# Optimization experiments

Hardware: AMD Instinct MI355X
Metric: run time of the kernel (lower is better)

## Reference

```python
import jax, jax.numpy as jnp
import numpy as np

D_MODEL = 1024
MAX_NUM_LAYERS = 4


def setup_inputs() -> dict:
    key = jax.random.key(0)
    ks = jax.random.split(key, 8)
    S, B, D, L = 1024, 2, D_MODEL, 3
    w = lambda k: (jax.random.normal(k, (D, D), dtype=jnp.float32) * 0.02)
    return {
        "x": jax.random.normal(ks[0], (S, B, D), dtype=jnp.float32),
        "layer_outputs": jax.random.normal(ks[1], (L, S, B, D), dtype=jnp.float32),
        "Wq": w(ks[2]), "bq": jnp.zeros((D,), jnp.float32),
        "Wk": w(ks[3]), "bk": jnp.zeros((D,), jnp.float32),
        "Wv": w(ks[4]), "bv": jnp.zeros((D,), jnp.float32),
        "Wo": w(ks[5]), "bo": jnp.zeros((D,), jnp.float32),
        "layer_weights": jnp.ones((MAX_NUM_LAYERS + 1,), jnp.float32),
        "num_heads": 16,
    }


def reference(x, layer_outputs, Wq, bq, Wk, bk, Wv, bv, Wo, bo, layer_weights, num_heads):
    # x: [S, B, D]; layer_outputs: [L, S, B, D] (stacked prev layer outputs)
    S, B, D = x.shape
    H = num_heads
    hd = D // H
    scale = hd ** -0.5
    # q from x only: [S, B*H, hd] -> [BH, S, hd]
    q = (x @ Wq.T + bq).reshape(S, B * H, hd).transpose(1, 0, 2)
    # k/v from x and all previous layer outputs (shared K/V projections)
    xs = jnp.concatenate([x[None], layer_outputs], axis=0)          # [Lp1, S, B, D]
    Lp1 = xs.shape[0]
    k = (xs @ Wk.T + bk).reshape(Lp1, S, B * H, hd).transpose(0, 2, 1, 3)  # [Lp1, BH, S, hd]
    v = (xs @ Wv.T + bv).reshape(Lp1, S, B * H, hd).transpose(0, 2, 1, 3)
    # per-layer scores, softmax over the key axis (torch dim=-2 of stacked scores)
    scores = jnp.einsum('bqd,lbkd->lbqk', q, k) * scale             # [Lp1, BH, S, S]
    attn = jax.nn.softmax(scores, axis=-1)
    lw = jax.nn.softmax(layer_weights[:Lp1])                        # [Lp1]
    combined = jnp.einsum('l,lbqk,lbkd->bqd', lw, attn, v)          # [BH, S, hd]
    combined = combined.transpose(1, 0, 2).reshape(S, B, D)
    return combined @ Wo.T + bo
```

## Files before the change

### kernel.cpp

```cpp
#include <hip/hip_runtime.h>
#include <hip/hip_bf16.h>
#include <math.h>

#define S_LEN   1024
#define BATCH   2
#define DMODEL  1024
#define NHEADS  16
#define HDIM    64
#define BHEADS  32
#define LP1     4
#define ROWS_PL 2048

typedef __attribute__((ext_vector_type(8)))  short bf16x8;
typedef __attribute__((ext_vector_type(4)))  float f32x4;
typedef __attribute__((ext_vector_type(16))) float f32x16;

__device__ inline ushort bf16_rne(float a) {
    unsigned u = __float_as_uint(a);
    return (ushort)((u + 0x7FFFu + ((u >> 16) & 1u)) >> 16);
}
__device__ inline float bf16_up(ushort h) { return __uint_as_float(((unsigned)h) << 16); }
__device__ inline void split_bf16(float a, ushort &hi, ushort &lo) {
    hi = bf16_rne(a);
    lo = bf16_rne(a - bf16_up(hi));
}
__device__ inline uint pk_bf16(float a, float b) {
    float2 f; f.x = a; f.y = b;
    __hip_bfloat162 h = __float22bfloat162_rn(f);
    return *reinterpret_cast<uint*>(&h);
}
#if __has_builtin(__builtin_amdgcn_exp2f)
__device__ inline float fast_exp2(float x) { return __builtin_amdgcn_exp2f(x); }
#else
__device__ inline float fast_exp2(float x) { return exp2f(x); }
#endif

__device__ inline void permswap(uint &a, uint &b) {
    asm("v_permlane32_swap_b32 %0, %1" : "+v"(a), "+v"(b));
}

__device__ inline void glds16(const ushort* g, ushort* l) {
    __builtin_amdgcn_global_load_lds(
        (const __attribute__((address_space(1))) void*)g,
        (__attribute__((address_space(3))) void*)l, 16, 0, 0);
}

#define SCLF 0.18033688011112042f

__global__ __launch_bounds__(256)
void presplit(const float* __restrict__ x, const float* __restrict__ lo,
              const float* __restrict__ Wq, const float* __restrict__ Wk,
              const float* __restrict__ Wv, const float* __restrict__ Wo,
              ushort* __restrict__ XsH, ushort* __restrict__ WH,
              ushort* __restrict__ WL)
{
    const int z = blockIdx.z;
    const float* src; ushort* dh; ushort* dl = nullptr; int n;
    if (z == 0)      { src = x;  dh = XsH;           n = 2097152; }
    else if (z == 1) { src = lo; dh = XsH + 2097152; n = 6291456; }
    else {
        const float* wsrc[4] = { Wq, Wk, Wv, Wo };
        src = wsrc[z - 2];
        dh = WH + (size_t)(z - 2) * 1048576;
        if (z == 2 || z == 5) dl = WL + (size_t)(z - 2) * 1048576;
        n = 1048576;
    }
    const int i = (blockIdx.x * 256 + threadIdx.x) * 8;
    if (i >= n) return;
    float v[8];
    *(float4*)&v[0] = *(const float4*)(src + i);
    *(float4*)&v[4] = *(const float4*)(src + i + 4);
    ushort h[8];
    #pragma unroll
    for (int j = 0; j < 8; ++j) h[j] = bf16_rne(v[j]);
    *(uint4*)(dh + i) = *(uint4*)h;
    if (dl) {
        ushort l[8];
        #pragma unroll
        for (int j = 0; j < 8; ++j) l[j] = bf16_rne(v[j] - bf16_up(h[j]));
        *(uint4*)(dl + i) = *(uint4*)l;
    }
}

template<int MODE>
__global__ __launch_bounds__(256)
void proj_g(const ushort* __restrict__ Abf,
            const ushort* __restrict__ Bhg, const ushort* __restrict__ Blg,
            const float* __restrict__ bias,
            float* __restrict__ outf, ushort* __restrict__ outh,
            ushort* __restrict__ outl)
{
    __shared__ ushort smem[3 * 2048];
    ushort* Ah = smem;
    ushort* Bh = smem + 2048;
    ushort* Bl = smem + 4096;

    const int fid = blockIdx.x;
    const int nt = (fid & 7) * 2 + ((fid >> 3) & 1);
    const int mt = fid >> 4;
    const int m0 = mt * 64, n0 = nt * 64;

    const int t  = threadIdx.x;
    const int wv = t >> 6, lane = t & 63;
    const int quad = lane >> 4, r = lane & 15;
    const int wm = wv & 1, wn = wv >> 1;
    const int mBase = wm * 32, nBase = wn * 32;

    const int lrow = lane >> 2;
    const int lch  = ((lane & 3) ^ (lrow & 3)) * 8;
    const ushort* Asrc  = Abf + (size_t)(m0 + wv * 16 + lrow) * DMODEL + lch;
    const ushort* Bhsrc = Bhg + (size_t)(n0 + wv * 16 + lrow) * DMODEL + lch;
    const ushort* Blsrc = Blg + (size_t)(n0 + wv * 16 + lrow) * DMODEL + lch;
    ushort* lA  = Ah + wv * 512;
    ushort* lBh = Bh + wv * 512;
    ushort* lBl = Bl + wv * 512;

    const int q0x = (quad ^ (r & 3)) << 3;
    f32x4 acc[2][2];
    #pragma unroll
    for (int i = 0; i < 2; ++i)
        #pragma unroll
        for (int j = 0; j < 2; ++j) acc[i][j] = (f32x4){0.f, 0.f, 0.f, 0.f};

    for (int k0 = 0; k0 < DMODEL; k0 += 32) {
        glds16(Asrc + k0, lA);
        glds16(Bhsrc + k0, lBh);
        glds16(Blsrc + k0, lBl);
        __syncthreads();
        bf16x8 fa[2], fbh[2], fbl[2];
        #pragma unroll
        for (int i = 0; i < 2; ++i)
            fa[i] = *(const bf16x8*)&Ah[(mBase + i * 16 + r) * 32 + q0x];
        #pragma unroll
        for (int j = 0; j < 2; ++j) {
            fbh[j] = *(const bf16x8*)&Bh[(nBase + j * 16 + r) * 32 + q0x];
            fbl[j] = *(const bf16x8*)&Bl[(nBase + j * 16 + r) * 32 + q0x];
        }
        #pragma unroll
        for (int i = 0; i < 2; ++i)
            #pragma unroll
            for (int j = 0; j < 2; ++j) {
                acc[i][j] = __builtin_amdgcn_mfma_f32_16x16x32_bf16(fa[i], fbh[j], acc[i][j], 0, 0, 0);
                acc[i][j] = __builtin_amdgcn_mfma_f32_16x16x32_bf16(fa[i], fbl[j], acc[i][j], 0, 0, 0);
            }
        __syncthreads();
    }

    const int cn = lane & 15;
    #pragma unroll
    for (int j = 0; j < 2; ++j) {
        const int n = n0 + nBase + j * 16 + cn;
        const float bv = bias[n];
        #pragma unroll
        for (int i = 0; i < 2; ++i) {
            const int mrow = m0 + mBase + i * 16 + quad * 4;
            #pragma unroll
            for (int g = 0; g < 4; ++g) {
                const int m = mrow + g;
                if (MODE == 1) {
                    outf[(size_t)m * DMODEL + n] = acc[i][j][g] + bv;
                } else {
                    const float val = (acc[i][j][g] + bv) * SCLF;
                    const int s = m >> 1, b = m & 1;
                    const int bh = b * 16 + (n >> 6), e = n & 63;
                    const size_t idx = (((size_t)bh * S_LEN) + s) * HDIM + e;
                    ushort hi, lov; split_bf16(val, hi, lov);
                    outh[idx] = hi; outl[idx] = lov;
                }
            }
        }
    }
}

__global__ __launch_bounds__(256, 4)
void proj_kv(const ushort* __restrict__ XsH,
             const ushort* __restrict__ KWh, const ushort* __restrict__ VWh,
             const float* __restrict__ bk, const float* __restrict__ bv,
             ushort* __restrict__ kout, ushort* __restrict__ vout)
{
    __shared__ ushort smem[10240];
    ushort* Ah = smem;
    ushort* Bp = smem + 2048;

    const int t  = threadIdx.x;
    const int m0 = blockIdx.y * 64, n0 = blockIdx.x * 128;
    const int lyr = m0 >> 11;

    const int wv = t >> 6, lane = t & 63;
    const int quad = lane >> 4, r = lane & 15;
    const int wm = wv & 1, wn = wv >> 1;
    const int mBase = wm * 32, nBase = wn * 64;

    const int lrow = lane >> 2;
    const int lch  = ((lane & 3) ^ (lrow & 3)) * 8;

    const ushort* Asrc = XsH + (size_t)(m0 + wv * 16 + lrow) * DMODEL + lch;
    const ushort* Bw[2] = { KWh, VWh };
    const ushort* Bsrc[2][2];
    #pragma unroll
    for (int p = 0; p < 2; ++p)
        #pragma unroll
        for (int seg = 0; seg < 2; ++seg)
            Bsrc[p][seg] = Bw[p] + (size_t)(n0 + wv * 32 + seg * 16 + lrow) * DMODEL + lch;

    const int q0x = (quad ^ (r & 3)) << 3;

    f32x4 aK[2][4], aV[2][4];
    #pragma unroll
    for (int i = 0; i < 2; ++i)
        #pragma unroll
        for (int j = 0; j < 4; ++j) {
            aK[i][j] = (f32x4){0.f, 0.f, 0.f, 0.f};
            aV[i][j] = (f32x4){0.f, 0.f, 0.f, 0.f};
        }

    for (int k0 = 0; k0 < DMODEL; k0 += 32) {
        glds16(Asrc + k0, Ah + wv * 512);
        #pragma unroll
        for (int p = 0; p < 2; ++p)
            #pragma unroll
            for (int seg = 0; seg < 2; ++seg)
                glds16(Bsrc[p][seg] + k0, Bp + p * 4096 + (wv * 2 + seg) * 512);
        __syncthreads();

        bf16x8 fa[2];
        #pragma unroll
        for (int i = 0; i < 2; ++i)
            fa[i] = *(const bf16x8*)&Ah[(mBase + i * 16 + r) * 32 + q0x];
        #pragma unroll
        for (int j = 0; j < 4; ++j) {
            const int off = (nBase + j * 16 + r) * 32 + q0x;
            const bf16x8 fkh = *(const bf16x8*)&Bp[off];
            const bf16x8 fvh = *(const bf16x8*)&Bp[4096 + off];
            #pragma unroll
            for (int i = 0; i < 2; ++i) {
                aK[i][j] = __builtin_amdgcn_mfma_f32_16x16x32_bf16(fa[i], fkh, aK[i][j], 0, 0, 0);
                aV[i][j] = __builtin_amdgcn_mfma_f32_16x16x32_bf16(fa[i], fvh, aV[i][j], 0, 0, 0);
            }
        }
        __syncthreads();
    }

    const int cn = lane & 15;

    #pragma unroll
    for (int j = 0; j < 4; ++j) {
        const int n = n0 + nBase + j * 16 + cn;
        const float bb = bk[n];
        const int e    = n & 63;
        const int es_k = e >> 4, half_k = (e >> 3) & 1, j_k = e & 7;
        const int h    = n >> 6;
        #pragma unroll
        for (int i = 0; i < 2; ++i) {
            #pragma unroll
            for (int g = 0; g < 4; ++g) {
                const int m = m0 + mBase + i * 16 + quad * 4 + g;
                const int rem = m & 2047, s = rem >> 1, b = rem & 1;
                const int bhI = lyr * 32 + b * 16 + h;
                const int kt  = s >> 5;
                const int lnk = half_k * 32 + (s & 31);
                kout[(size_t)bhI * 65536 + (size_t)(kt * 4 + es_k) * 512 + lnk * 8 + j_k]
                    = bf16_rne(aK[i][j][g] + bb);
            }
        }
    }

    ushort* T = smem;
    __syncthreads();
    #pragma unroll
    for (int j = 0; j < 4; ++j) {
        const int nloc = nBase + j * 16 + cn;
        const float bb = bv[n0 + nloc];
        #pragma unroll
        for (int i = 0; i < 2; ++i) {
            #pragma unroll
            for (int g = 0; g < 4; ++g) {
                const int mloc = mBase + i * 16 + quad * 4 + g;
                T[nloc * 66 + mloc] = bf16_rne(aV[i][j][g] + bb);
            }
        }
    }
    __syncthreads();
    {
        const int nloc = t >> 1, bsel = t & 1;
        const int n = n0 + nloc, h = n >> 6;
        const int e = n & 63;
        const int dg = e >> 5, lid_v = e & 31;
        const int s0g = (m0 & 2047) >> 1;
        const int kt  = s0g >> 5;
        const int bhI = lyr * 32 + bsel * 16 + h;
        ushort* dstb = vout + (size_t)bhI * 65536 + (size_t)kt * 2048;
        #pragma unroll
        for (int c = 0; c < 4; ++c) {
            ushort tmp[8];
            #pragma unroll
            for (int j = 0; j < 8; ++j)
                tmp[j] = T[nloc * 66 + 2 * (c * 8 + j) + bsel];
            const int ks = c >> 1, hv = c & 1;
            *(uint4*)(dstb + (ks * 2 + dg) * 512 + (hv * 32 + lid_v) * 8) = *(uint4*)tmp;
        }
    }
}

__global__ __launch_bounds__(256, 2)
void attn_mfma(const ushort* __restrict__ qhg, const ushort* __restrict__ qlg,
               const ushort* __restrict__ kh, const ushort* __restrict__ vth,
               const float* __restrict__ lwraw, float* __restrict__ part)
{
    const int t    = threadIdx.x;
    const int wv   = t >> 6, lane = t & 63;
    const int half = lane >> 5, lid = lane & 31;

    const int fid  = blockIdx.x;
    const int xcd  = fid & 7, slot = fid >> 3;
    const int pair = xcd * 16 + (slot >> 2);
    const int qt   = slot & 3;
    const int bh   = pair & 31, l = pair >> 5;
    const int qbase = qt * 256 + wv * 64;

    float wl;
    {
        float v[LP1], wm = -3.0e38f;
        #pragma unroll
        for (int i = 0; i < LP1; ++i) { v[i] = lwraw[i]; wm = fmaxf(wm, v[i]); }
        float ws = 0.f;
        #pragma unroll
        for (int i = 0; i < LP1; ++i) { v[i] = __expf(v[i] - wm); ws += v[i]; }
        wl = v[l] / ws;
    }

    bf16x8 qh[2][4], ql[2][4];
    #pragma unroll
    for (int u = 0; u < 2; ++u) {
        const size_t qoff = ((size_t)bh * S_LEN + qbase + u * 32 + lid) * HDIM + half * 8;
        #pragma unroll
        for (int es = 0; es < 4; ++es) {
            qh[u][es] = *(const bf16x8*)(qhg + qoff + es * 16);
            ql[u][es] = *(const bf16x8*)(qlg + qoff + es * 16);
        }
    }

    f32x16 o[2][2];
    #pragma unroll
    for (int u = 0; u < 2; ++u)
        #pragma unroll
        for (int dg = 0; dg < 2; ++dg)
            #pragma unroll
            for (int i = 0; i < 16; ++i) o[u][dg][i] = 0.f;
    float ls[2] = {0.f, 0.f};

    const size_t kvo = (size_t)(l * BHEADS + bh) * S_LEN * HDIM;
    const ushort* kfb = kh  + kvo + (size_t)lane * 8;
    const ushort* vfb = vth + kvo + (size_t)lane * 8;

    bf16x8 kb[4], kn[4];
    #pragma unroll
    for (int es = 0; es < 4; ++es)
        kb[es] = *(const bf16x8*)(kfb + es * 512);
    #pragma unroll
    for (int es = 0; es < 4; ++es)
        kn[es] = *(const bf16x8*)(kfb + 2048 + es * 512);

    f32x16 sa[2];
    #pragma unroll
    for (int u = 0; u < 2; ++u)
        #pragma unroll
        for (int i = 0; i < 16; ++i) sa[u][i] = 0.f;
    #pragma unroll
    for (int es = 0; es < 4; ++es)
        #pragma unroll
        for (int u = 0; u < 2; ++u) {
            sa[u] = __builtin_amdgcn_mfma_f32_32x32x16_bf16(kb[es], qh[u][es], sa[u], 0, 0, 0);
            sa[u] = __builtin_amdgcn_mfma_f32_32x32x16_bf16(kb[es], ql[u][es], sa[u], 0, 0, 0);
        }

    for (int kt = 0; kt < 32; ++kt) {
        bf16x8 vb[2][2];
        {
            const ushort* vp = vfb + (size_t)kt * 2048;
            #pragma unroll
            for (int ks = 0; ks < 2; ++ks)
                #pragma unroll
                for (int dg = 0; dg < 2; ++dg)
                    vb[ks][dg] = *(const bf16x8*)(vp + (ks * 2 + dg) * 512);
        }

        bf16x8 pf[2][2];
        #pragma unroll
        for (int ks = 0; ks < 2; ++ks) {
            #pragma unroll
            for (int u = 0; u < 2; ++u) {
                const float p0 = fast_exp2(sa[u][8 * ks + 0]);
                const float p1 = fast_exp2(sa[u][8 * ks + 1]);
                const float p2 = fast_exp2(sa[u][8 * ks + 2]);
                const float p3 = fast_exp2(sa[u][8 * ks + 3]);
                const float p4 = fast_exp2(sa[u][8 * ks + 4]);
                const float p5 = fast_exp2(sa[u][8 * ks + 5]);
                const float p6 = fast_exp2(sa[u][8 * ks + 6]);
                const float p7 = fast_exp2(sa[u][8 * ks + 7]);
                ls[u] += ((p0 + p1) + (p2 + p3)) + ((p4 + p5) + (p6 + p7));

                uint a0 = pk_bf16(p0, p1);
                uint a1 = pk_bf16(p2, p3);
                uint b0 = pk_bf16(p4, p5);
                uint b1 = pk_bf16(p6, p7);
                permswap(a0, b0);
                permswap(a1, b1);
                union { uint w[4]; bf16x8 v; } pu;
                pu.w[0] = a0; pu.w[1] = a1; pu.w[2] = b0; pu.w[3] = b1;
                pf[ks][u] = pu.v;
            }
        }

        #pragma unroll
        for (int es = 0; es < 4; ++es) kb[es] = kn[es];
        {
            const ushort* kp = kfb + (size_t)((kt + 2) & 31) * 2048;
            #pragma unroll
            for (int es = 0; es < 4; ++es) kn[es] = *(const bf16x8*)(kp + es * 512);
        }

        #pragma unroll
        for (int u = 0; u < 2; ++u)
            #pragma unroll
            for (int i = 0; i < 16; ++i) sa[u][i] = 0.f;
        __builtin_amdgcn_s_setprio(1);
        #pragma unroll
        for (int es = 0; es < 4; ++es)
            #pragma unroll
            for (int u = 0; u < 2; ++u) {
                sa[u] = __builtin_amdgcn_mfma_f32_32x32x16_bf16(kb[es], qh[u][es], sa[u], 0, 0, 0);
                sa[u] = __builtin_amdgcn_mfma_f32_32x32x16_bf16(kb[es], ql[u][es], sa[u], 0, 0, 0);
            }
        __builtin_amdgcn_s_setprio(0);

        __builtin_amdgcn_s_setprio(1);
        #pragma unroll
        for (int ks = 0; ks < 2; ++ks)
            #pragma unroll
            for (int dg = 0; dg < 2; ++dg)
                #pragma unroll
                for (int u = 0; u < 2; ++u)
                    o[u][dg] = __builtin_amdgcn_mfma_f32_32x32x16_bf16(vb[ks][dg], pf[ks][u], o[u][dg], 0, 0, 0);
        __builtin_amdgcn_s_setprio(0);
    }

    const int b = bh >> 4, hh = bh & 15;
    #pragma unroll
    for (int u = 0; u < 2; ++u) {
        float lsv = ls[u];
        lsv += __shfl_xor(lsv, 32);
        const float sc = wl / lsv;
        const int q = qbase + u * 32 + lid;
        float* pb = part + (size_t)l * (ROWS_PL * DMODEL)
                  + ((size_t)q * BATCH + b) * DMODEL + hh * HDIM;
        #pragma unroll
        for (int dg = 0; dg < 2; ++dg)
            #pragma unroll
            for (int rq = 0; rq < 4; ++rq) {
                float4 vv;
                vv.x = o[u][dg][rq * 4 + 0] * sc;
                vv.y = o[u][dg][rq * 4 + 1] * sc;
                vv.z = o[u][dg][rq * 4 + 2] * sc;
                vv.w = o[u][dg][rq * 4 + 3] * sc;
                *(float4*)(pb + dg * 32 + rq * 8 + half * 4) = vv;
            }
    }
}

__global__ __launch_bounds__(256)
void sum_y(const float* __restrict__ part, ushort* __restrict__ YH)
{
    const int i = (blockIdx.x * 256 + threadIdx.x) * 8;
    float acc[8];
    #pragma unroll
    for (int c = 0; c < 2; ++c) {
        float4 s = *(const float4*)(part + i + c * 4);
        #pragma unroll
        for (int l = 1; l < LP1; ++l) {
            const float4 p = *(const float4*)(part + (size_t)l * 2097152 + i + c * 4);
            s.x += p.x; s.y += p.y; s.z += p.z; s.w += p.w;
        }
        acc[c * 4 + 0] = s.x; acc[c * 4 + 1] = s.y;
        acc[c * 4 + 2] = s.z; acc[c * 4 + 3] = s.w;
    }
    uint out[4];
    #pragma unroll
    for (int c = 0; c < 4; ++c) out[c] = pk_bf16(acc[c * 2], acc[c * 2 + 1]);
    *(uint4*)(YH + i) = *(uint4*)out;
}

extern "C" void kernel_launch(void* const* d_in, const int* in_sizes, int n_in,
                              void* d_out, int out_size, void* d_ws, size_t ws_size,
                              hipStream_t stream) {
    const float* x  = (const float*)d_in[0];
    const float* lo = (const float*)d_in[1];
    const float* Wq = (const float*)d_in[2];
    const float* bq = (const float*)d_in[3];
    const float* Wk = (const float*)d_in[4];
    const float* bk = (const float*)d_in[5];
    const float* Wv = (const float*)d_in[6];
    const float* bv = (const float*)d_in[7];
    const float* Wo = (const float*)d_in[8];
    const float* bo = (const float*)d_in[9];
    const float* lw = (const float*)d_in[10];
    float* out = (float*)d_out;

    char* ws = (char*)d_ws;
    ushort* XsH  = (ushort*)(ws);
    ushort* WH   = (ushort*)(ws + 16777216);
    ushort* WL   = (ushort*)(ws + 25165824);
    ushort* qhb  = (ushort*)(ws + 33554432);
    ushort* qlb  = (ushort*)(ws + 37748736);
    ushort* khb  = (ushort*)(ws + 41943040);
    ushort* vthb = (ushort*)(ws + 58720256);
    float*  part = (float*)(ws + 75497472);
    ushort* YH   = (ushort*)(ws + 109051904);

    dim3 blk(256);
    presplit<<<dim3(3072, 1, 6), blk, 0, stream>>>(x, lo, Wq, Wk, Wv, Wo, XsH, WH, WL);
    proj_g<0><<<dim3(512), blk, 0, stream>>>(XsH, WH, WL, bq, nullptr, qhb, qlb);
    proj_kv<<<dim3(8, 128), blk, 0, stream>>>(XsH,
        WH + 1048576, WH + 2097152, bk, bv, khb, vthb);
    attn_mfma<<<dim3(512), blk, 0, stream>>>(qhb, qlb, khb, vthb, lw, part);
    sum_y<<<dim3(1024), blk, 0, stream>>>(part, YH);
    proj_g<1><<<dim3(512), blk, 0, stream>>>(YH, WH + 3145728, WL + 3145728, bo, out, nullptr, nullptr);
}
```

Measured before the change: 259.0 us.

## Double-buffer LDS tiles in projection GEMMs and zero-init scores via MFMA operand

Both projection kernels now keep two LDS stage buffers. The next K-slice is issued into the alternate buffer while MFMAs consume the current one, which removes one barrier per iteration and overlaps global-to-LDS loads with compute. The attention kernel no longer zeroes its score accumulators with explicit moves and instead feeds a zero vector as the accumulator of the first MFMA in each chain. The price is doubled LDS per block (40 KB for proj_kv), which may lower occupancy against the launch bound of 4, plus a held zero register vector.

```diff
diff --git a/kernel.cpp b/kernel.cpp
--- a/kernel.cpp
+++ b/kernel.cpp
@@ -90,10 +90,7 @@
             float* __restrict__ outf, ushort* __restrict__ outh,
             ushort* __restrict__ outl)
 {
-    __shared__ ushort smem[3 * 2048];
-    ushort* Ah = smem;
-    ushort* Bh = smem + 2048;
-    ushort* Bl = smem + 4096;
+    __shared__ ushort smem[2][3 * 2048];
 
     const int fid = blockIdx.x;
     const int nt = (fid & 7) * 2 + ((fid >> 3) & 1);
@@ -111,9 +108,6 @@
     const ushort* Asrc  = Abf + (size_t)(m0 + wv * 16 + lrow) * DMODEL + lch;
     const ushort* Bhsrc = Bhg + (size_t)(n0 + wv * 16 + lrow) * DMODEL + lch;
     const ushort* Blsrc = Blg + (size_t)(n0 + wv * 16 + lrow) * DMODEL + lch;
-    ushort* lA  = Ah + wv * 512;
-    ushort* lBh = Bh + wv * 512;
-    ushort* lBl = Bl + wv * 512;
 
     const int q0x = (quad ^ (r & 3)) << 3;
     f32x4 acc[2][2];
@@ -122,11 +116,22 @@
         #pragma unroll
         for (int j = 0; j < 2; ++j) acc[i][j] = (f32x4){0.f, 0.f, 0.f, 0.f};
 
-    for (int k0 = 0; k0 < DMODEL; k0 += 32) {
-        glds16(Asrc + k0, lA);
-        glds16(Bhsrc + k0, lBh);
-        glds16(Blsrc + k0, lBl);
+    glds16(Asrc,  smem[0]        + wv * 512);
+    glds16(Bhsrc, smem[0] + 2048 + wv * 512);
+    glds16(Blsrc, smem[0] + 4096 + wv * 512);
+
+    for (int k = 0; k < 32; ++k) {
+        const int cur = k & 1;
         __syncthreads();
+        if (k + 1 < 32) {
+            const int off = (k + 1) * 32;
+            glds16(Asrc  + off, smem[cur ^ 1]        + wv * 512);
+            glds16(Bhsrc + off, smem[cur ^ 1] + 2048 + wv * 512);
+            glds16(Blsrc + off, smem[cur ^ 1] + 4096 + wv * 512);
+        }
+        const ushort* Ah = smem[cur];
+        const ushort* Bh = smem[cur] + 2048;
+        const ushort* Bl = smem[cur] + 4096;
         bf16x8 fa[2], fbh[2], fbl[2];
         #pragma unroll
         for (int i = 0; i < 2; ++i)
@@ -143,7 +148,6 @@
                 acc[i][j] = __builtin_amdgcn_mfma_f32_16x16x32_bf16(fa[i], fbh[j], acc[i][j], 0, 0, 0);
                 acc[i][j] = __builtin_amdgcn_mfma_f32_16x16x32_bf16(fa[i], fbl[j], acc[i][j], 0, 0, 0);
             }
-        __syncthreads();
     }
 
     const int cn = lane & 15;
@@ -178,9 +182,7 @@
              const float* __restrict__ bk, const float* __restrict__ bv,
              ushort* __restrict__ kout, ushort* __restrict__ vout)
 {
-    __shared__ ushort smem[10240];
-    ushort* Ah = smem;
-    ushort* Bp = smem + 2048;
+    __shared__ ushort smem[2][10240];
 
     const int t  = threadIdx.x;
     const int m0 = blockIdx.y * 64, n0 = blockIdx.x * 128;
@@ -214,14 +216,28 @@
             aV[i][j] = (f32x4){0.f, 0.f, 0.f, 0.f};
         }
 
-    for (int k0 = 0; k0 < DMODEL; k0 += 32) {
-        glds16(Asrc + k0, Ah + wv * 512);
-        #pragma unroll
-        for (int p = 0; p < 2; ++p)
-            #pragma unroll
-            for (int seg = 0; seg < 2; ++seg)
-                glds16(Bsrc[p][seg] + k0, Bp + p * 4096 + (wv * 2 + seg) * 512);
+    glds16(Asrc, smem[0] + wv * 512);
+    #pragma unroll
+    for (int p = 0; p < 2; ++p)
+        #pragma unroll
+        for (int seg = 0; seg < 2; ++seg)
+            glds16(Bsrc[p][seg], smem[0] + 2048 + p * 4096 + (wv * 2 + seg) * 512);
+
+    for (int k = 0; k < 32; ++k) {
+        const int cur = k & 1;
         __syncthreads();
+        if (k + 1 < 32) {
+            const int off = (k + 1) * 32;
+            glds16(Asrc + off, smem[cur ^ 1] + wv * 512);
+            #pragma unroll
+            for (int p = 0; p < 2; ++p)
+                #pragma unroll
+                for (int seg = 0; seg < 2; ++seg)
+                    glds16(Bsrc[p][seg] + off,
+                           smem[cur ^ 1] + 2048 + p * 4096 + (wv * 2 + seg) * 512);
+        }
+        const ushort* Ah = smem[cur];
+        const ushort* Bp = smem[cur] + 2048;
 
         bf16x8 fa[2];
         #pragma unroll
@@ -238,7 +254,6 @@
                 aV[i][j] = __builtin_amdgcn_mfma_f32_16x16x32_bf16(fa[i], fvh, aV[i][j], 0, 0, 0);
             }
         }
-        __syncthreads();
     }
 
     const int cn = lane & 15;
@@ -265,7 +280,7 @@
         }
     }
 
-    ushort* T = smem;
+    ushort* T = smem[0];
     __syncthreads();
     #pragma unroll
     for (int j = 0; j < 4; ++j) {
@@ -349,6 +364,10 @@
             for (int i = 0; i < 16; ++i) o[u][dg][i] = 0.f;
     float ls[2] = {0.f, 0.f};
 
+    f32x16 zf;
+    #pragma unroll
+    for (int i = 0; i < 16; ++i) zf[i] = 0.f;
+
     const size_t kvo = (size_t)(l * BHEADS + bh) * S_LEN * HDIM;
     const ushort* kfb = kh  + kvo + (size_t)lane * 8;
     const ushort* vfb = vth + kvo + (size_t)lane * 8;
@@ -363,14 +382,11 @@
 
     f32x16 sa[2];
     #pragma unroll
-    for (int u = 0; u < 2; ++u)
-        #pragma unroll
-        for (int i = 0; i < 16; ++i) sa[u][i] = 0.f;
-    #pragma unroll
     for (int es = 0; es < 4; ++es)
         #pragma unroll
         for (int u = 0; u < 2; ++u) {
-            sa[u] = __builtin_amdgcn_mfma_f32_32x32x16_bf16(kb[es], qh[u][es], sa[u], 0, 0, 0);
+            sa[u] = __builtin_amdgcn_mfma_f32_32x32x16_bf16(kb[es], qh[u][es],
+                                                            es == 0 ? zf : sa[u], 0, 0, 0);
             sa[u] = __builtin_amdgcn_mfma_f32_32x32x16_bf16(kb[es], ql[u][es], sa[u], 0, 0, 0);
         }
 
@@ -420,16 +436,13 @@
             for (int es = 0; es < 4; ++es) kn[es] = *(const bf16x8*)(kp + es * 512);
         }
 
-        #pragma unroll
-        for (int u = 0; u < 2; ++u)
-            #pragma unroll
-            for (int i = 0; i < 16; ++i) sa[u][i] = 0.f;
         __builtin_amdgcn_s_setprio(1);
         #pragma unroll
         for (int es = 0; es < 4; ++es)
             #pragma unroll
             for (int u = 0; u < 2; ++u) {
-                sa[u] = __builtin_amdgcn_mfma_f32_32x32x16_bf16(kb[es], qh[u][es], sa[u], 0, 0, 0);
+                sa[u] = __builtin_amdgcn_mfma_f32_32x32x16_bf16(kb[es], qh[u][es],
+                                                                es == 0 ? zf : sa[u], 0, 0, 0);
                 sa[u] = __builtin_amdgcn_mfma_f32_32x32x16_bf16(kb[es], ql[u][es], sa[u], 0, 0, 0);
             }
         __builtin_amdgcn_s_setprio(0);
```

New measurement: 248.4 us. 1.04x faster.
